# Kernel optimization log

Hardware: AMD Instinct MI355X
Metric: run time of the kernel (lower is better)

## Reference

```python
import jax, jax.numpy as jnp
import numpy as np

N, K, D = 32768, 8192, 256


def setup_inputs() -> dict:
    key = jax.random.key(0)
    k1, k2 = jax.random.split(key)
    x = jax.random.normal(k1, (N, D), dtype=jnp.float32)
    vectors = jax.random.normal(k2, (K, D), dtype=jnp.float32)  # codebook
    return {"x": x, "vectors": vectors}


def reference(x, vectors):
    # torch.cdist(x[:,None,:], vectors[None]) followed by argmin over K.
    # Euclidean distance is monotone in squared distance, so argmin over the
    # without a sqrt, matching the original math exactly for the returned ids.
    x2 = jnp.sum(x * x, axis=-1, keepdims=True)          # [N, 1]
    c2 = jnp.sum(vectors * vectors, axis=-1)             # [K]
    d2 = x2 + c2 - 2.0 * jnp.matmul(x, vectors.T)        # [N, K]
    indices = jnp.argmin(d2, axis=-1)                    # [N]
    return indices.astype(jnp.int32)
```

## Files before the change

### kernel.cpp

```cpp
#include <hip/hip_runtime.h>
#include <stdint.h>
#include <stddef.h>


#define N_PTS 32768
#define K_CB  8192
#define D_DIM 256
#define TM 128
#define TN 128
#define SPLITK 4
#define KCHUNK (K_CB / SPLITK)
#define NTILES (KCHUNK / TN)

#define WS_XH   0
#define WS_XL   (WS_XH + N_PTS * D_DIM * 2)
#define WS_CH   (WS_XL + N_PTS * D_DIM * 2)
#define WS_CL   (WS_CH + K_CB * D_DIM * 2)
#define WS_C2   (WS_CL + K_CB * D_DIM * 2)
#define WS_PD   (WS_C2 + K_CB * 4)
#define WS_PI   (WS_PD + SPLITK * N_PTS * 4)
#define WS_END  (WS_PI + SPLITK * N_PTS * 4)

typedef _Float16 half4v __attribute__((ext_vector_type(4)));
typedef _Float16 half8v __attribute__((ext_vector_type(8)));
typedef float    f32x4  __attribute__((ext_vector_type(4)));

__device__ __forceinline__ void gld16(const void* g, void* l) {
    __builtin_amdgcn_global_load_lds(
        (const __attribute__((address_space(1))) void*)g,
        (__attribute__((address_space(3))) void*)l, 16, 0, 0);
}


__global__ void __launch_bounds__(256)
split_kernel(const float* __restrict__ src, _Float16* __restrict__ h_out,
             _Float16* __restrict__ l_out) {
    const int i = blockIdx.x * 256 + threadIdx.x;
    const float4 v = ((const float4*)src)[i];
    half4v h = {(_Float16)v.x, (_Float16)v.y, (_Float16)v.z, (_Float16)v.w};
    half4v l = {(_Float16)((v.x - (float)h[0]) * 2048.0f),
                (_Float16)((v.y - (float)h[1]) * 2048.0f),
                (_Float16)((v.z - (float)h[2]) * 2048.0f),
                (_Float16)((v.w - (float)h[3]) * 2048.0f)};
    *(half4v*)(h_out + (size_t)i * 4) = h;
    *(half4v*)(l_out + (size_t)i * 4) = l;
}

__global__ void __launch_bounds__(256)
cnorms_kernel(const float* __restrict__ vecs, float* __restrict__ c2) {
    int gwave = (blockIdx.x * 256 + threadIdx.x) >> 6;
    int lane  = threadIdx.x & 63;
    const float* src = vecs + (size_t)gwave * D_DIM;
    float4 v = ((const float4*)src)[lane];
    float s = v.x * v.x + v.y * v.y + v.z * v.z + v.w * v.w;
#pragma unroll
    for (int off = 32; off > 0; off >>= 1) s += __shfl_down(s, off, 64);
    if (lane == 0) c2[gwave] = s;
}


__global__ void __launch_bounds__(256, 2)
vq_main_fast(const _Float16* __restrict__ xh_g, const _Float16* __restrict__ xl_g,
             const _Float16* __restrict__ ch_g, const _Float16* __restrict__ cl_g,
             const float* __restrict__ c2, float* __restrict__ pd, int* __restrict__ pi) {
    __shared__ __align__(16) char lds[65536];

    const int t    = threadIdx.x;
    const int lane = t & 63;
    const int wv   = t >> 6;
    const int wy   = wv >> 1, wx = wv & 1;
    const int fr   = lane & 15;
    const int g    = lane >> 4;

    const int split = blockIdx.x & (SPLITK - 1);
    const int pbase = (blockIdx.x >> 2) * TM;
    const int kbase = split * KCHUNK;

    const int rowoff = (lane >> 3) * (D_DIM * 2) + (((lane & 7) ^ (lane >> 3)) << 4);
    const char* xh_w = (const char*)xh_g + (size_t)(pbase + wv * 32) * (D_DIM * 2) + rowoff;
    const char* xl_w = (const char*)xl_g + (size_t)(pbase + wv * 32) * (D_DIM * 2) + rowoff;
    char* ldsA_h = lds +         (wv * 32) * 128;
    char* ldsA_l = lds + 16384 + (wv * 32) * 128;
    char* ldsB_h = lds + 32768 + (wv * 32) * 128;
    char* ldsB_l = lds + 49152 + (wv * 32) * 128;

    int aoff[4][2], boff[4][2];
#pragma unroll
    for (int i = 0; i < 4; ++i)
#pragma unroll
        for (int ks = 0; ks < 2; ++ks) {
            aoff[i][ks] = (wy * 64 + i * 16 + fr) * 128 + (((ks * 4 + g) ^ (fr & 7)) << 4);
            boff[i][ks] = 32768 + (wx * 64 + i * 16 + fr) * 128 + (((ks * 4 + g) ^ (fr & 7)) << 4);
        }

    float best[16];
    int   bidx[16];
#pragma unroll
    for (int i = 0; i < 16; ++i) { best[i] = 3.4e38f; bidx[i] = 0; }

    for (int kt = 0; kt < NTILES; ++kt) {
        const int ktbase = kbase + kt * TN;
        const char* ch_w = (const char*)ch_g + (size_t)(ktbase + wv * 32) * (D_DIM * 2) + rowoff;
        const char* cl_w = (const char*)cl_g + (size_t)(ktbase + wv * 32) * (D_DIM * 2) + rowoff;

        f32x4 acc[4][4];
#pragma unroll
        for (int i = 0; i < 4; ++i)
#pragma unroll
            for (int j = 0; j < 4; ++j) {
                f32x4 z = {0.f, 0.f, 0.f, 0.f};
                acc[i][j] = z;
            }

#pragma unroll 1
        for (int dkc = 0; dkc < 4; ++dkc) {
            const int gofs = dkc * 128;
            __syncthreads();
#pragma unroll
            for (int q = 0; q < 4; ++q) {
                gld16(xh_w + q * 4096 + gofs, ldsA_h + q * 1024);
                gld16(xl_w + q * 4096 + gofs, ldsA_l + q * 1024);
                gld16(ch_w + q * 4096 + gofs, ldsB_h + q * 1024);
                gld16(cl_w + q * 4096 + gofs, ldsB_l + q * 1024);
            }
            __syncthreads();
#pragma unroll
            for (int ks = 0; ks < 2; ++ks) {
                half8v a1[4], a2[4], a3[4];
#pragma unroll
                for (int i = 0; i < 4; ++i) {
                    const char* p = lds + aoff[i][ks];
                    a1[i] = *(const half8v*)p;
                    a3[i] = *(const half8v*)(p + 16384);
                    a2[i] = a1[i] * (_Float16)4.8828125e-4f;
                }
#pragma unroll
                for (int j = 0; j < 4; ++j) {
                    const char* p = lds + boff[j][ks];
                    half8v b1 = *(const half8v*)p;
                    half8v b2 = *(const half8v*)(p + 16384);
                    half8v b3 = b1 * (_Float16)4.8828125e-4f;
#pragma unroll
                    for (int i = 0; i < 4; ++i) {
                        acc[i][j] = __builtin_amdgcn_mfma_f32_16x16x32_f16(a1[i], b1, acc[i][j], 0, 0, 0);
                        acc[i][j] = __builtin_amdgcn_mfma_f32_16x16x32_f16(a2[i], b2, acc[i][j], 0, 0, 0);
                        acc[i][j] = __builtin_amdgcn_mfma_f32_16x16x32_f16(a3[i], b3, acc[i][j], 0, 0, 0);
                    }
                }
            }
        }

#pragma unroll
        for (int j = 0; j < 4; ++j) {
            const int cg = ktbase + wx * 64 + j * 16 + fr;
            const float c2v = c2[cg];
#pragma unroll
            for (int i = 0; i < 4; ++i)
#pragma unroll
                for (int r = 0; r < 4; ++r) {
                    const float v = fmaf(-2.0f, acc[i][j][r], c2v);
                    const int s = i * 4 + r;
                    if (v < best[s]) { best[s] = v; bidx[s] = cg; }
                }
        }
    }

    __syncthreads();
    float* rd = (float*)lds;
    int*   ri = (int*)lds + 256;
#pragma unroll
    for (int i = 0; i < 4; ++i)
#pragma unroll
        for (int r = 0; r < 4; ++r) {
            float bv = best[i * 4 + r];
            int   bi = bidx[i * 4 + r];
#pragma unroll
            for (int off = 1; off < 16; off <<= 1) {
                const float ov = __shfl_xor(bv, off, 64);
                const int   oi = __shfl_xor(bi, off, 64);
                if (ov < bv || (ov == bv && oi < bi)) { bv = ov; bi = oi; }
            }
            if (fr == 0) {
                const int rowl = wy * 64 + i * 16 + g * 4 + r;
                rd[rowl * 2 + wx] = bv;
                ri[rowl * 2 + wx] = bi;
            }
        }
    __syncthreads();
    if (t < TM) {
        float b0 = rd[t * 2];
        int   i0 = ri[t * 2];
        const float b1 = rd[t * 2 + 1];
        const int   i1 = ri[t * 2 + 1];
        if (b1 < b0 || (b1 == b0 && i1 < i0)) { b0 = b1; i0 = i1; }
        pd[split * N_PTS + pbase + t] = b0;
        pi[split * N_PTS + pbase + t] = i0;
    }
}


#define BK 32
#define LS (BK + 4)

__device__ inline half8v load8(const _Float16* p) {
    half4v a = *(const half4v*)p;
    half4v b = *(const half4v*)(p + 4);
    return __builtin_shufflevector(a, b, 0, 1, 2, 3, 4, 5, 6, 7);
}

struct Trip { _Float16 h, s2, l2; };

__device__ inline Trip cvt3(float v) {
    Trip t;
    _Float16 hh = (_Float16)v;
    float hf = (float)hh;
    t.h  = hh;
    t.s2 = (_Float16)(hf * 4.8828125e-4f);
    t.l2 = (_Float16)((v - hf) * 2048.0f);
    return t;
}

__global__ void __launch_bounds__(256, 2)
vq_main_v3(const float* __restrict__ x, const float* __restrict__ vecs,
           const float* __restrict__ c2, float* __restrict__ pd, int* __restrict__ pi) {
    __shared__ _Float16 lds[6 * TM * LS];
    _Float16* xh  = lds;
    _Float16* xs2 = lds + 1 * TM * LS;
    _Float16* xl2 = lds + 2 * TM * LS;
    _Float16* ch  = lds + 3 * TM * LS;
    _Float16* cl2 = lds + 4 * TM * LS;
    _Float16* cs2 = lds + 5 * TM * LS;

    const int t     = threadIdx.x;
    const int split = blockIdx.x & (SPLITK - 1);
    const int pbase = (blockIdx.x >> 2) * TM;
    const int kbase = split * KCHUNK;

    const int lane = t & 63;
    const int wv   = t >> 6;
    const int wy   = wv >> 1, wx = wv & 1;
    const int fr   = lane & 15;
    const int g    = lane >> 4;
    const int kb   = g * 8;

    const int srow = t >> 3;
    const int sc4  = (t & 7) * 4;

    float best[16];
    int   bidx[16];
#pragma unroll
    for (int i = 0; i < 16; ++i) { best[i] = 3.4e38f; bidx[i] = 0; }

    for (int kt = 0; kt < NTILES; ++kt) {
        const int ktbase = kbase + kt * TN;
        f32x4 acc[4][4];
#pragma unroll
        for (int i = 0; i < 4; ++i)
#pragma unroll
            for (int j = 0; j < 4; ++j) {
                f32x4 z = {0.f, 0.f, 0.f, 0.f};
                acc[i][j] = z;
            }
        for (int dk = 0; dk < D_DIM; dk += BK) {
            __syncthreads();
#pragma unroll
            for (int p = 0; p < 4; ++p) {
                const int row = srow + p * 32;
                const float4 v = *(const float4*)&x[(size_t)(pbase + row) * D_DIM + dk + sc4];
                const Trip t0 = cvt3(v.x), t1 = cvt3(v.y), t2 = cvt3(v.z), t3 = cvt3(v.w);
                half4v h  = {t0.h,  t1.h,  t2.h,  t3.h};
                half4v s2 = {t0.s2, t1.s2, t2.s2, t3.s2};
                half4v l2 = {t0.l2, t1.l2, t2.l2, t3.l2};
                *(half4v*)&xh [row * LS + sc4] = h;
                *(half4v*)&xs2[row * LS + sc4] = s2;
                *(half4v*)&xl2[row * LS + sc4] = l2;
                const float4 w = *(const float4*)&vecs[(size_t)(ktbase + row) * D_DIM + dk + sc4];
                const Trip u0 = cvt3(w.x), u1 = cvt3(w.y), u2 = cvt3(w.z), u3 = cvt3(w.w);
                half4v hc = {u0.h,  u1.h,  u2.h,  u3.h};
                half4v sc = {u0.s2, u1.s2, u2.s2, u3.s2};
                half4v lc = {u0.l2, u1.l2, u2.l2, u3.l2};
                *(half4v*)&ch [row * LS + sc4] = hc;
                *(half4v*)&cs2[row * LS + sc4] = sc;
                *(half4v*)&cl2[row * LS + sc4] = lc;
            }
            __syncthreads();
            half8v a1[4], a2[4], a3[4], b1[4], b2[4], b3[4];
#pragma unroll
            for (int i = 0; i < 4; ++i) {
                const int aoff = (wy * 64 + i * 16 + fr) * LS + kb;
                a1[i] = load8(&xh [aoff]);
                a2[i] = load8(&xs2[aoff]);
                a3[i] = load8(&xl2[aoff]);
                const int boff2 = (wx * 64 + i * 16 + fr) * LS + kb;
                b1[i] = load8(&ch [boff2]);
                b2[i] = load8(&cl2[boff2]);
                b3[i] = load8(&cs2[boff2]);
            }
#pragma unroll
            for (int i = 0; i < 4; ++i)
#pragma unroll
                for (int j = 0; j < 4; ++j) {
                    acc[i][j] = __builtin_amdgcn_mfma_f32_16x16x32_f16(a1[i], b1[j], acc[i][j], 0, 0, 0);
                    acc[i][j] = __builtin_amdgcn_mfma_f32_16x16x32_f16(a2[i], b2[j], acc[i][j], 0, 0, 0);
                    acc[i][j] = __builtin_amdgcn_mfma_f32_16x16x32_f16(a3[i], b3[j], acc[i][j], 0, 0, 0);
                }
        }
#pragma unroll
        for (int j = 0; j < 4; ++j) {
            const int cg = ktbase + wx * 64 + j * 16 + fr;
            const float c2v = c2[cg];
#pragma unroll
            for (int i = 0; i < 4; ++i)
#pragma unroll
                for (int r = 0; r < 4; ++r) {
                    const float v = fmaf(-2.0f, acc[i][j][r], c2v);
                    const int s = i * 4 + r;
                    if (v < best[s]) { best[s] = v; bidx[s] = cg; }
                }
        }
    }
    __syncthreads();
    float* rd = (float*)lds;
    int*   ri = (int*)lds + 256;
#pragma unroll
    for (int i = 0; i < 4; ++i)
#pragma unroll
        for (int r = 0; r < 4; ++r) {
            float bv = best[i * 4 + r];
            int   bi = bidx[i * 4 + r];
#pragma unroll
            for (int off = 1; off < 16; off <<= 1) {
                const float ov = __shfl_xor(bv, off, 64);
                const int   oi = __shfl_xor(bi, off, 64);
                if (ov < bv || (ov == bv && oi < bi)) { bv = ov; bi = oi; }
            }
            if (fr == 0) {
                const int rowl = wy * 64 + i * 16 + g * 4 + r;
                rd[rowl * 2 + wx] = bv;
                ri[rowl * 2 + wx] = bi;
            }
        }
    __syncthreads();
    if (t < TM) {
        float b0 = rd[t * 2];
        int   i0 = ri[t * 2];
        const float b1 = rd[t * 2 + 1];
        const int   i1 = ri[t * 2 + 1];
        if (b1 < b0 || (b1 == b0 && i1 < i0)) { b0 = b1; i0 = i1; }
        pd[split * N_PTS + pbase + t] = b0;
        pi[split * N_PTS + pbase + t] = i0;
    }
}


__global__ void __launch_bounds__(256)
vq_combine(const float* __restrict__ pd, const int* __restrict__ pi,
           int* __restrict__ out) {
    const int p = blockIdx.x * 256 + threadIdx.x;
    float bb = pd[p];
    int   bi = pi[p];
#pragma unroll
    for (int s = 1; s < SPLITK; ++s) {
        const float v  = pd[s * N_PTS + p];
        const int   vi = pi[s * N_PTS + p];
        if (v < bb || (v == bb && vi < bi)) { bb = v; bi = vi; }
    }
    out[p] = bi;
}

extern "C" void kernel_launch(void* const* d_in, const int* in_sizes, int n_in,
                              void* d_out, int out_size, void* d_ws, size_t ws_size,
                              hipStream_t stream) {
    const float* x    = (const float*)d_in[0];
    const float* vecs = (const float*)d_in[1];
    int* out = (int*)d_out;
    char* ws = (char*)d_ws;

    if (ws_size >= (size_t)WS_END) {
        _Float16* xh = (_Float16*)(ws + WS_XH);
        _Float16* xl = (_Float16*)(ws + WS_XL);
        _Float16* ch = (_Float16*)(ws + WS_CH);
        _Float16* cl = (_Float16*)(ws + WS_CL);
        float* c2 = (float*)(ws + WS_C2);
        float* pd = (float*)(ws + WS_PD);
        int*   pi = (int*)(ws + WS_PI);

        hipLaunchKernelGGL(split_kernel, dim3(N_PTS * D_DIM / 4 / 256), dim3(256), 0, stream,
                           x, xh, xl);
        hipLaunchKernelGGL(split_kernel, dim3(K_CB * D_DIM / 4 / 256), dim3(256), 0, stream,
                           vecs, ch, cl);
        hipLaunchKernelGGL(cnorms_kernel, dim3(K_CB / 4), dim3(256), 0, stream,
                           vecs, c2);
        hipLaunchKernelGGL(vq_main_fast, dim3((N_PTS / TM) * SPLITK), dim3(256), 0, stream,
                           xh, xl, ch, cl, c2, pd, pi);
        hipLaunchKernelGGL(vq_combine, dim3(N_PTS / 256), dim3(256), 0, stream,
                           pd, pi, out);
    } else {
        float* c2 = (float*)ws;
        float* pd = (float*)ws + K_CB;
        int*   pi = (int*)((float*)ws + K_CB + SPLITK * N_PTS);
        hipLaunchKernelGGL(cnorms_kernel, dim3(K_CB / 4), dim3(256), 0, stream,
                           vecs, c2);
        hipLaunchKernelGGL(vq_main_v3, dim3((N_PTS / TM) * SPLITK), dim3(256), 0, stream,
                           x, vecs, c2, pd, pi);
        hipLaunchKernelGGL(vq_combine, dim3(N_PTS / 256), dim3(256), 0, stream,
                           pd, pi, out);
    }
}
```

Before: 482.9 us.

## Double-buffer LDS staging in main VQ kernel and fuse prep kernels

The main kernel now stages smaller 32-wide D chunks into two 32KB LDS buffers. It issues the async global-to-LDS loads for the next chunk while MFMAs run on the current one, instead of syncing, loading, then computing. The swizzle is dropped in favour of a plain 64-byte row layout, which may cause LDS bank conflicts. The two split kernels and the codebook norm kernel are merged into one prep launch to cut launch overhead.

```diff
diff --git a/kernel.cpp b/kernel.cpp
--- a/kernel.cpp
+++ b/kernel.cpp
@@ -11,6 +11,7 @@
 #define SPLITK 4
 #define KCHUNK (K_CB / SPLITK)
 #define NTILES (KCHUNK / TN)
+#define NCHUNKS (NTILES * 8)
 
 #define WS_XH   0
 #define WS_XL   (WS_XH + N_PTS * D_DIM * 2)
@@ -32,18 +33,40 @@
 }
 
 
+#define XBLOCKS (N_PTS * D_DIM / 4 / 256)
+#define CBLOCKS (K_CB * D_DIM / 4 / 256)
+
 __global__ void __launch_bounds__(256)
-split_kernel(const float* __restrict__ src, _Float16* __restrict__ h_out,
-             _Float16* __restrict__ l_out) {
-    const int i = blockIdx.x * 256 + threadIdx.x;
-    const float4 v = ((const float4*)src)[i];
-    half4v h = {(_Float16)v.x, (_Float16)v.y, (_Float16)v.z, (_Float16)v.w};
-    half4v l = {(_Float16)((v.x - (float)h[0]) * 2048.0f),
-                (_Float16)((v.y - (float)h[1]) * 2048.0f),
-                (_Float16)((v.z - (float)h[2]) * 2048.0f),
-                (_Float16)((v.w - (float)h[3]) * 2048.0f)};
-    *(half4v*)(h_out + (size_t)i * 4) = h;
-    *(half4v*)(l_out + (size_t)i * 4) = l;
+prep_kernel(const float* __restrict__ x, const float* __restrict__ vecs,
+            _Float16* __restrict__ xh, _Float16* __restrict__ xl,
+            _Float16* __restrict__ ch, _Float16* __restrict__ cl,
+            float* __restrict__ c2) {
+    const int b = blockIdx.x;
+    if (b < XBLOCKS) {
+        const int i = b * 256 + threadIdx.x;
+        const float4 v = ((const float4*)x)[i];
+        half4v h = {(_Float16)v.x, (_Float16)v.y, (_Float16)v.z, (_Float16)v.w};
+        half4v l = {(_Float16)((v.x - (float)h[0]) * 2048.0f),
+                    (_Float16)((v.y - (float)h[1]) * 2048.0f),
+                    (_Float16)((v.z - (float)h[2]) * 2048.0f),
+                    (_Float16)((v.w - (float)h[3]) * 2048.0f)};
+        *(half4v*)(xh + (size_t)i * 4) = h;
+        *(half4v*)(xl + (size_t)i * 4) = l;
+    } else {
+        const int i = (b - XBLOCKS) * 256 + threadIdx.x;
+        const float4 v = ((const float4*)vecs)[i];
+        half4v h = {(_Float16)v.x, (_Float16)v.y, (_Float16)v.z, (_Float16)v.w};
+        half4v l = {(_Float16)((v.x - (float)h[0]) * 2048.0f),
+                    (_Float16)((v.y - (float)h[1]) * 2048.0f),
+                    (_Float16)((v.z - (float)h[2]) * 2048.0f),
+                    (_Float16)((v.w - (float)h[3]) * 2048.0f)};
+        *(half4v*)(ch + (size_t)i * 4) = h;
+        *(half4v*)(cl + (size_t)i * 4) = l;
+        float s = v.x * v.x + v.y * v.y + v.z * v.z + v.w * v.w;
+#pragma unroll
+        for (int off = 32; off > 0; off >>= 1) s += __shfl_down(s, off, 64);
+        if ((threadIdx.x & 63) == 0) c2[i >> 6] = s;
+    }
 }
 
 __global__ void __launch_bounds__(256)
@@ -76,34 +99,68 @@
     const int pbase = (blockIdx.x >> 2) * TM;
     const int kbase = split * KCHUNK;
 
-    const int rowoff = (lane >> 3) * (D_DIM * 2) + (((lane & 7) ^ (lane >> 3)) << 4);
-    const char* xh_w = (const char*)xh_g + (size_t)(pbase + wv * 32) * (D_DIM * 2) + rowoff;
-    const char* xl_w = (const char*)xl_g + (size_t)(pbase + wv * 32) * (D_DIM * 2) + rowoff;
-    char* ldsA_h = lds +         (wv * 32) * 128;
-    char* ldsA_l = lds + 16384 + (wv * 32) * 128;
-    char* ldsB_h = lds + 32768 + (wv * 32) * 128;
-    char* ldsB_l = lds + 49152 + (wv * 32) * 128;
-
-    int aoff[4][2], boff[4][2];
-#pragma unroll
-    for (int i = 0; i < 4; ++i)
-#pragma unroll
-        for (int ks = 0; ks < 2; ++ks) {
-            aoff[i][ks] = (wy * 64 + i * 16 + fr) * 128 + (((ks * 4 + g) ^ (fr & 7)) << 4);
-            boff[i][ks] = 32768 + (wx * 64 + i * 16 + fr) * 128 + (((ks * 4 + g) ^ (fr & 7)) << 4);
-        }
+    const int srowoff = (lane >> 2) * (D_DIM * 2) + ((lane & 3) << 4);
+    const char* xh_s = (const char*)xh_g + (size_t)(pbase + wv * 32) * (D_DIM * 2) + srowoff;
+    const char* xl_s = (const char*)xl_g + (size_t)(pbase + wv * 32) * (D_DIM * 2) + srowoff;
+    const char* ch_s = (const char*)ch_g + (size_t)(kbase + wv * 32) * (D_DIM * 2) + srowoff;
+    const char* cl_s = (const char*)cl_g + (size_t)(kbase + wv * 32) * (D_DIM * 2) + srowoff;
+    const int stA = wv * 32 * 64;
+
+    int aoff[4], boff[4];
+#pragma unroll
+    for (int i = 0; i < 4; ++i) {
+        aoff[i] = (wy * 64 + i * 16 + fr) * 64 + (g << 4);
+        boff[i] = 16384 + (wx * 64 + i * 16 + fr) * 64 + (g << 4);
+    }
+
+    f32x4 acc[4][4];
+
+    auto STAGE = [&](char* L, int c) {
+        const size_t kofs = (size_t)(c >> 3) * (TN * D_DIM * 2);
+        const int gofs = (c & 7) * 64;
+#pragma unroll
+        for (int q = 0; q < 2; ++q) {
+            gld16(xh_s + q * 8192 + gofs, L +         stA + q * 1024);
+            gld16(xl_s + q * 8192 + gofs, L +  8192 + stA + q * 1024);
+            gld16(ch_s + kofs + q * 8192 + gofs, L + 16384 + stA + q * 1024);
+            gld16(cl_s + kofs + q * 8192 + gofs, L + 24576 + stA + q * 1024);
+        }
+    };
+
+    auto COMPUTE = [&](const char* L) {
+        half8v a1[4], a2[4], a3[4];
+#pragma unroll
+        for (int i = 0; i < 4; ++i) {
+            const char* p = L + aoff[i];
+            a1[i] = *(const half8v*)p;
+            a3[i] = *(const half8v*)(p + 8192);
+            a2[i] = a1[i] * (_Float16)4.8828125e-4f;
+        }
+#pragma unroll
+        for (int j = 0; j < 4; ++j) {
+            const char* p = L + boff[j];
+            half8v b1 = *(const half8v*)p;
+            half8v b2 = *(const half8v*)(p + 8192);
+            half8v b3 = b1 * (_Float16)4.8828125e-4f;
+#pragma unroll
+            for (int i = 0; i < 4; ++i) {
+                acc[i][j] = __builtin_amdgcn_mfma_f32_16x16x32_f16(a1[i], b1, acc[i][j], 0, 0, 0);
+                acc[i][j] = __builtin_amdgcn_mfma_f32_16x16x32_f16(a2[i], b2, acc[i][j], 0, 0, 0);
+                acc[i][j] = __builtin_amdgcn_mfma_f32_16x16x32_f16(a3[i], b3, acc[i][j], 0, 0, 0);
+            }
+        }
+    };
 
     float best[16];
     int   bidx[16];
 #pragma unroll
     for (int i = 0; i < 16; ++i) { best[i] = 3.4e38f; bidx[i] = 0; }
 
+    STAGE(lds, 0);
+    __syncthreads();
+
+#pragma unroll 1
     for (int kt = 0; kt < NTILES; ++kt) {
-        const int ktbase = kbase + kt * TN;
-        const char* ch_w = (const char*)ch_g + (size_t)(ktbase + wv * 32) * (D_DIM * 2) + rowoff;
-        const char* cl_w = (const char*)cl_g + (size_t)(ktbase + wv * 32) * (D_DIM * 2) + rowoff;
-
-        f32x4 acc[4][4];
 #pragma unroll
         for (int i = 0; i < 4; ++i)
 #pragma unroll
@@ -113,43 +170,17 @@
             }
 
 #pragma unroll 1
-        for (int dkc = 0; dkc < 4; ++dkc) {
-            const int gofs = dkc * 128;
+        for (int du = 0; du < 4; ++du) {
+            const int c = kt * 8 + du * 2;
+            if (c + 1 < NCHUNKS) STAGE(lds + 32768, c + 1);
+            COMPUTE(lds);
             __syncthreads();
-#pragma unroll
-            for (int q = 0; q < 4; ++q) {
-                gld16(xh_w + q * 4096 + gofs, ldsA_h + q * 1024);
-                gld16(xl_w + q * 4096 + gofs, ldsA_l + q * 1024);
-                gld16(ch_w + q * 4096 + gofs, ldsB_h + q * 1024);
-                gld16(cl_w + q * 4096 + gofs, ldsB_l + q * 1024);
-            }
+            if (c + 2 < NCHUNKS) STAGE(lds, c + 2);
+            COMPUTE(lds + 32768);
             __syncthreads();
-#pragma unroll
-            for (int ks = 0; ks < 2; ++ks) {
-                half8v a1[4], a2[4], a3[4];
-#pragma unroll
-                for (int i = 0; i < 4; ++i) {
-                    const char* p = lds + aoff[i][ks];
-                    a1[i] = *(const half8v*)p;
-                    a3[i] = *(const half8v*)(p + 16384);
-                    a2[i] = a1[i] * (_Float16)4.8828125e-4f;
-                }
-#pragma unroll
-                for (int j = 0; j < 4; ++j) {
-                    const char* p = lds + boff[j][ks];
-                    half8v b1 = *(const half8v*)p;
-                    half8v b2 = *(const half8v*)(p + 16384);
-                    half8v b3 = b1 * (_Float16)4.8828125e-4f;
-#pragma unroll
-                    for (int i = 0; i < 4; ++i) {
-                        acc[i][j] = __builtin_amdgcn_mfma_f32_16x16x32_f16(a1[i], b1, acc[i][j], 0, 0, 0);
-                        acc[i][j] = __builtin_amdgcn_mfma_f32_16x16x32_f16(a2[i], b2, acc[i][j], 0, 0, 0);
-                        acc[i][j] = __builtin_amdgcn_mfma_f32_16x16x32_f16(a3[i], b3, acc[i][j], 0, 0, 0);
-                    }
-                }
-            }
-        }
-
+        }
+
+        const int ktbase = kbase + kt * TN;
 #pragma unroll
         for (int j = 0; j < 4; ++j) {
             const int cg = ktbase + wx * 64 + j * 16 + fr;
@@ -385,12 +416,8 @@
         float* pd = (float*)(ws + WS_PD);
         int*   pi = (int*)(ws + WS_PI);
 
-        hipLaunchKernelGGL(split_kernel, dim3(N_PTS * D_DIM / 4 / 256), dim3(256), 0, stream,
-                           x, xh, xl);
-        hipLaunchKernelGGL(split_kernel, dim3(K_CB * D_DIM / 4 / 256), dim3(256), 0, stream,
-                           vecs, ch, cl);
-        hipLaunchKernelGGL(cnorms_kernel, dim3(K_CB / 4), dim3(256), 0, stream,
-                           vecs, c2);
+        hipLaunchKernelGGL(prep_kernel, dim3(XBLOCKS + CBLOCKS), dim3(256), 0, stream,
+                           x, vecs, xh, xl, ch, cl, c2);
         hipLaunchKernelGGL(vq_main_fast, dim3((N_PTS / TM) * SPLITK), dim3(256), 0, stream,
                            xh, xl, ch, cl, c2, pd, pi);
         hipLaunchKernelGGL(vq_combine, dim3(N_PTS / 256), dim3(256), 0, stream,
```

After: 554.7 us. +14.9%, slower.

## Switch main kernel to 32x32x16 MFMA tiles and fuse prep kernels

Applied to the files above, without the earlier changes.

The main distance kernel now uses 32x32x16 f16 MFMA instructions on 2x2 tiles per wave instead of 16x16x32 on 4x4 tiles. This halves the number of LDS fragment loads per K step and uses the larger MFMA shape for higher throughput per instruction. The argmin bookkeeping grows to 32 rows per lane, which raises register pressure, and the reduction is updated to the 32-lane layout. Separately, the x and codebook split kernels and the codebook-norm kernel are merged into one launch to cut launch overhead and avoid reading the codebook twice.

```diff
diff --git a/kernel.cpp b/kernel.cpp
--- a/kernel.cpp
+++ b/kernel.cpp
@@ -21,9 +21,10 @@
 #define WS_PI   (WS_PD + SPLITK * N_PTS * 4)
 #define WS_END  (WS_PI + SPLITK * N_PTS * 4)
 
-typedef _Float16 half4v __attribute__((ext_vector_type(4)));
-typedef _Float16 half8v __attribute__((ext_vector_type(8)));
-typedef float    f32x4  __attribute__((ext_vector_type(4)));
+typedef _Float16 half4v  __attribute__((ext_vector_type(4)));
+typedef _Float16 half8v  __attribute__((ext_vector_type(8)));
+typedef float    f32x4   __attribute__((ext_vector_type(4)));
+typedef float    f32x16  __attribute__((ext_vector_type(16)));
 
 __device__ __forceinline__ void gld16(const void* g, void* l) {
     __builtin_amdgcn_global_load_lds(
@@ -32,18 +33,40 @@
 }
 
 
+#define XBLOCKS (N_PTS * D_DIM / 4 / 256)
+#define CBLOCKS (K_CB * D_DIM / 4 / 256)
+
 __global__ void __launch_bounds__(256)
-split_kernel(const float* __restrict__ src, _Float16* __restrict__ h_out,
-             _Float16* __restrict__ l_out) {
-    const int i = blockIdx.x * 256 + threadIdx.x;
-    const float4 v = ((const float4*)src)[i];
-    half4v h = {(_Float16)v.x, (_Float16)v.y, (_Float16)v.z, (_Float16)v.w};
-    half4v l = {(_Float16)((v.x - (float)h[0]) * 2048.0f),
-                (_Float16)((v.y - (float)h[1]) * 2048.0f),
-                (_Float16)((v.z - (float)h[2]) * 2048.0f),
-                (_Float16)((v.w - (float)h[3]) * 2048.0f)};
-    *(half4v*)(h_out + (size_t)i * 4) = h;
-    *(half4v*)(l_out + (size_t)i * 4) = l;
+prep_kernel(const float* __restrict__ x, const float* __restrict__ vecs,
+            _Float16* __restrict__ xh, _Float16* __restrict__ xl,
+            _Float16* __restrict__ ch, _Float16* __restrict__ cl,
+            float* __restrict__ c2) {
+    const int b = blockIdx.x;
+    if (b < XBLOCKS) {
+        const int i = b * 256 + threadIdx.x;
+        const float4 v = ((const float4*)x)[i];
+        half4v h = {(_Float16)v.x, (_Float16)v.y, (_Float16)v.z, (_Float16)v.w};
+        half4v l = {(_Float16)((v.x - (float)h[0]) * 2048.0f),
+                    (_Float16)((v.y - (float)h[1]) * 2048.0f),
+                    (_Float16)((v.z - (float)h[2]) * 2048.0f),
+                    (_Float16)((v.w - (float)h[3]) * 2048.0f)};
+        *(half4v*)(xh + (size_t)i * 4) = h;
+        *(half4v*)(xl + (size_t)i * 4) = l;
+    } else {
+        const int i = (b - XBLOCKS) * 256 + threadIdx.x;
+        const float4 v = ((const float4*)vecs)[i];
+        half4v h = {(_Float16)v.x, (_Float16)v.y, (_Float16)v.z, (_Float16)v.w};
+        half4v l = {(_Float16)((v.x - (float)h[0]) * 2048.0f),
+                    (_Float16)((v.y - (float)h[1]) * 2048.0f),
+                    (_Float16)((v.z - (float)h[2]) * 2048.0f),
+                    (_Float16)((v.w - (float)h[3]) * 2048.0f)};
+        *(half4v*)(ch + (size_t)i * 4) = h;
+        *(half4v*)(cl + (size_t)i * 4) = l;
+        float s = v.x * v.x + v.y * v.y + v.z * v.z + v.w * v.w;
+#pragma unroll
+        for (int off = 32; off > 0; off >>= 1) s += __shfl_down(s, off, 64);
+        if ((threadIdx.x & 63) == 0) c2[i >> 6] = s;
+    }
 }
 
 __global__ void __launch_bounds__(256)
@@ -69,8 +92,9 @@
     const int lane = t & 63;
     const int wv   = t >> 6;
     const int wy   = wv >> 1, wx = wv & 1;
-    const int fr   = lane & 15;
-    const int g    = lane >> 4;
+    const int cr   = lane & 31;
+    const int hi   = lane >> 5;
+    const int sx   = cr & 7;
 
     const int split = blockIdx.x & (SPLITK - 1);
     const int pbase = (blockIdx.x >> 2) * TM;
@@ -84,33 +108,28 @@
     char* ldsB_h = lds + 32768 + (wv * 32) * 128;
     char* ldsB_l = lds + 49152 + (wv * 32) * 128;
 
-    int aoff[4][2], boff[4][2];
-#pragma unroll
-    for (int i = 0; i < 4; ++i)
-#pragma unroll
-        for (int ks = 0; ks < 2; ++ks) {
-            aoff[i][ks] = (wy * 64 + i * 16 + fr) * 128 + (((ks * 4 + g) ^ (fr & 7)) << 4);
-            boff[i][ks] = 32768 + (wx * 64 + i * 16 + fr) * 128 + (((ks * 4 + g) ^ (fr & 7)) << 4);
-        }
-
-    float best[16];
-    int   bidx[16];
-#pragma unroll
-    for (int i = 0; i < 16; ++i) { best[i] = 3.4e38f; bidx[i] = 0; }
+    int arow[2], brow[2];
+#pragma unroll
+    for (int ti = 0; ti < 2; ++ti) arow[ti] = (wy * 64 + ti * 32 + cr) * 128;
+#pragma unroll
+    for (int tj = 0; tj < 2; ++tj) brow[tj] = 32768 + (wx * 64 + tj * 32 + cr) * 128;
+
+    float best[32];
+    int   bidx[32];
+#pragma unroll
+    for (int i = 0; i < 32; ++i) { best[i] = 3.4e38f; bidx[i] = 0; }
 
     for (int kt = 0; kt < NTILES; ++kt) {
         const int ktbase = kbase + kt * TN;
         const char* ch_w = (const char*)ch_g + (size_t)(ktbase + wv * 32) * (D_DIM * 2) + rowoff;
         const char* cl_w = (const char*)cl_g + (size_t)(ktbase + wv * 32) * (D_DIM * 2) + rowoff;
 
-        f32x4 acc[4][4];
-#pragma unroll
-        for (int i = 0; i < 4; ++i)
-#pragma unroll
-            for (int j = 0; j < 4; ++j) {
-                f32x4 z = {0.f, 0.f, 0.f, 0.f};
-                acc[i][j] = z;
-            }
+        f32x16 acc[2][2];
+#pragma unroll
+        for (int ti = 0; ti < 2; ++ti)
+#pragma unroll
+            for (int tj = 0; tj < 2; ++tj)
+                acc[ti][tj] = (f32x16)(0.0f);
 
 #pragma unroll 1
         for (int dkc = 0; dkc < 4; ++dkc) {
@@ -125,41 +144,42 @@
             }
             __syncthreads();
 #pragma unroll
-            for (int ks = 0; ks < 2; ++ks) {
-                half8v a1[4], a2[4], a3[4];
-#pragma unroll
-                for (int i = 0; i < 4; ++i) {
-                    const char* p = lds + aoff[i][ks];
-                    a1[i] = *(const half8v*)p;
-                    a3[i] = *(const half8v*)(p + 16384);
-                    a2[i] = a1[i] * (_Float16)4.8828125e-4f;
+            for (int ks2 = 0; ks2 < 4; ++ks2) {
+                const int slot = ((ks2 * 2 + hi) ^ sx) << 4;
+                half8v a1[2], a2[2], a3[2];
+#pragma unroll
+                for (int ti = 0; ti < 2; ++ti) {
+                    const char* p = lds + arow[ti] + slot;
+                    a1[ti] = *(const half8v*)p;
+                    a3[ti] = *(const half8v*)(p + 16384);
+                    a2[ti] = a1[ti] * (_Float16)4.8828125e-4f;
                 }
 #pragma unroll
-                for (int j = 0; j < 4; ++j) {
-                    const char* p = lds + boff[j][ks];
+                for (int tj = 0; tj < 2; ++tj) {
+                    const char* p = lds + brow[tj] + slot;
                     half8v b1 = *(const half8v*)p;
                     half8v b2 = *(const half8v*)(p + 16384);
                     half8v b3 = b1 * (_Float16)4.8828125e-4f;
 #pragma unroll
-                    for (int i = 0; i < 4; ++i) {
-                        acc[i][j] = __builtin_amdgcn_mfma_f32_16x16x32_f16(a1[i], b1, acc[i][j], 0, 0, 0);
-                        acc[i][j] = __builtin_amdgcn_mfma_f32_16x16x32_f16(a2[i], b2, acc[i][j], 0, 0, 0);
-                        acc[i][j] = __builtin_amdgcn_mfma_f32_16x16x32_f16(a3[i], b3, acc[i][j], 0, 0, 0);
+                    for (int ti = 0; ti < 2; ++ti) {
+                        acc[ti][tj] = __builtin_amdgcn_mfma_f32_32x32x16_f16(a1[ti], b1, acc[ti][tj], 0, 0, 0);
+                        acc[ti][tj] = __builtin_amdgcn_mfma_f32_32x32x16_f16(a2[ti], b2, acc[ti][tj], 0, 0, 0);
+                        acc[ti][tj] = __builtin_amdgcn_mfma_f32_32x32x16_f16(a3[ti], b3, acc[ti][tj], 0, 0, 0);
                     }
                 }
             }
         }
 
 #pragma unroll
-        for (int j = 0; j < 4; ++j) {
-            const int cg = ktbase + wx * 64 + j * 16 + fr;
+        for (int tj = 0; tj < 2; ++tj) {
+            const int cg = ktbase + wx * 64 + tj * 32 + cr;
             const float c2v = c2[cg];
 #pragma unroll
-            for (int i = 0; i < 4; ++i)
-#pragma unroll
-                for (int r = 0; r < 4; ++r) {
-                    const float v = fmaf(-2.0f, acc[i][j][r], c2v);
-                    const int s = i * 4 + r;
+            for (int ti = 0; ti < 2; ++ti)
+#pragma unroll
+                for (int r = 0; r < 16; ++r) {
+                    const float v = fmaf(-2.0f, acc[ti][tj][r], c2v);
+                    const int s = ti * 16 + r;
                     if (v < best[s]) { best[s] = v; bidx[s] = cg; }
                 }
         }
@@ -169,19 +189,19 @@
     float* rd = (float*)lds;
     int*   ri = (int*)lds + 256;
 #pragma unroll
-    for (int i = 0; i < 4; ++i)
-#pragma unroll
-        for (int r = 0; r < 4; ++r) {
-            float bv = best[i * 4 + r];
-            int   bi = bidx[i * 4 + r];
-#pragma unroll
-            for (int off = 1; off < 16; off <<= 1) {
+    for (int ti = 0; ti < 2; ++ti)
+#pragma unroll
+        for (int r = 0; r < 16; ++r) {
+            float bv = best[ti * 16 + r];
+            int   bi = bidx[ti * 16 + r];
+#pragma unroll
+            for (int off = 1; off < 32; off <<= 1) {
                 const float ov = __shfl_xor(bv, off, 64);
                 const int   oi = __shfl_xor(bi, off, 64);
                 if (ov < bv || (ov == bv && oi < bi)) { bv = ov; bi = oi; }
             }
-            if (fr == 0) {
-                const int rowl = wy * 64 + i * 16 + g * 4 + r;
+            if (cr == 0) {
+                const int rowl = wy * 64 + ti * 32 + (r & 3) + 8 * (r >> 2) + 4 * hi;
                 rd[rowl * 2 + wx] = bv;
                 ri[rowl * 2 + wx] = bi;
             }
@@ -385,12 +405,8 @@
         float* pd = (float*)(ws + WS_PD);
         int*   pi = (int*)(ws + WS_PI);
 
-        hipLaunchKernelGGL(split_kernel, dim3(N_PTS * D_DIM / 4 / 256), dim3(256), 0, stream,
-                           x, xh, xl);
-        hipLaunchKernelGGL(split_kernel, dim3(K_CB * D_DIM / 4 / 256), dim3(256), 0, stream,
-                           vecs, ch, cl);
-        hipLaunchKernelGGL(cnorms_kernel, dim3(K_CB / 4), dim3(256), 0, stream,
-                           vecs, c2);
+        hipLaunchKernelGGL(prep_kernel, dim3(XBLOCKS + CBLOCKS), dim3(256), 0, stream,
+                           x, vecs, xh, xl, ch, cl, c2);
         hipLaunchKernelGGL(vq_main_fast, dim3((N_PTS / TM) * SPLITK), dim3(256), 0, stream,
                            xh, xl, ch, cl, c2, pd, pi);
         hipLaunchKernelGGL(vq_combine, dim3(N_PTS / 256), dim3(256), 0, stream,
```

Result: slower. 516.8 us (+7.0%).
